# Kernel tuning notes

Measured on AMD Instinct MI355X. Metric: run time of the kernel, lower is better.

## Reference

```python
import jax, jax.numpy as jnp
import numpy as np
import math

H = 1024
N_HEADS = 16
B, S = 2, 2048

def setup_inputs() -> dict:
    key = jax.random.key(0)
    ks = jax.random.split(key, 10)
    s = 0.02
    inp = {
        "x": jax.random.normal(ks[0], (B, S, H), dtype=jnp.float32),
        "attention_mask": jnp.zeros((B, 1, 1, S), dtype=jnp.float32),
        "Wq": jax.random.normal(ks[1], (H, H), dtype=jnp.float32) * s,
        "bq": jnp.zeros((H,), dtype=jnp.float32),
        "Wk": jax.random.normal(ks[2], (H, H), dtype=jnp.float32) * s,
        "bk": jnp.zeros((H,), dtype=jnp.float32),
        "Wv": jax.random.normal(ks[3], (H, H), dtype=jnp.float32) * s,
        "bv": jnp.zeros((H,), dtype=jnp.float32),
        "Wo": jax.random.normal(ks[4], (H, H), dtype=jnp.float32) * s,
        "bo": jnp.zeros((H,), dtype=jnp.float32),
    }
    return inp

def reference(x, attention_mask, Wq, bq, Wk, bk, Wv, bv, Wo, bo):
    b, s, h = x.shape
    n = N_HEADS
    d = h // n
    scale = 1.0 / math.sqrt(h / n)
    # Linear projections (torch Linear: x @ W.T + b)
    q = (x @ Wq.T + bq).reshape(b, s, n, d).transpose(0, 2, 1, 3)  # [b,n,s,d]
    k = (x @ Wk.T + bk).reshape(b, s, n, d).transpose(0, 2, 1, 3)
    v = (x @ Wv.T + bv).reshape(b, s, n, d).transpose(0, 2, 1, 3)
    scores = jnp.einsum("bnqd,bnkd->bnqk", q, k) * scale + attention_mask
    probs = jax.nn.softmax(scores, axis=-1)
    attn = jnp.einsum("bnqk,bnkd->bnqd", probs, v)
    attn = attn.transpose(0, 2, 1, 3).reshape(b, s, h)
    return attn @ Wo.T + bo
```

## Files before the change

### kernel.cpp

```cpp
#include <hip/hip_runtime.h>

typedef __bf16 bf16;
typedef __bf16 bf16x8 __attribute__((ext_vector_type(8)));
typedef __bf16 bf16x4 __attribute__((ext_vector_type(4)));
typedef float f32x4 __attribute__((ext_vector_type(4)));
typedef float f32x16 __attribute__((ext_vector_type(16)));
typedef unsigned int u32;
typedef u32 u32x4 __attribute__((ext_vector_type(4)));
typedef const u32 __attribute__((address_space(1)))* gp1_t;
typedef u32 __attribute__((address_space(3)))* lp3_t;

constexpr int Hdim = 1024;
constexpr int SEQ  = 2048;
constexpr int NB   = 2;
constexpr int NHEAD = 16;
constexpr int DHEAD = 64;
constexpr int MR = NB * SEQ;
constexpr float LOG2E = 1.4426950408889634f;
constexpr float QSCALE = 0.125f * LOG2E;

__device__ __forceinline__ float fexp2(float x) { return __builtin_amdgcn_exp2f(x); }

__device__ __forceinline__ void gld16(const void* g, void* l) {
  __builtin_amdgcn_global_load_lds((gp1_t)g, (lp3_t)l, 16, 0, 0);
}

__device__ __forceinline__ u32 cvtpk_bf16(float lo, float hi) {
  u32 r;
  asm("v_cvt_pk_bf16_f32 %0, %1, %2" : "=v"(r) : "v"(lo), "v"(hi));
  return r;
}

__global__ __launch_bounds__(256) void cvt_all_k(
    const float* __restrict__ x, const float* __restrict__ Wq, const float* __restrict__ Wk,
    const float* __restrict__ Wv, const float* __restrict__ Wo, const float* __restrict__ mask,
    bf16* __restrict__ xb, bf16* __restrict__ wqkv, bf16* __restrict__ wob,
    bf16* __restrict__ maskB) {
  const int n8x = MR * Hdim / 8;
  const int n8w = Hdim * Hdim / 8;
  int i = blockIdx.x * 256 + threadIdx.x;
  const float* src;
  bf16* dst;
  int slot;
  if (i < n8x) {
    src = x; dst = xb; slot = i;
  } else if (i < n8x + 4 * n8w) {
    int j = i - n8x;
    int w = j >> 17;
    int o = j & (n8w - 1);
    if (w == 0)      { src = Wq; dst = wqkv;            }
    else if (w == 1) { src = Wk; dst = wqkv + (size_t)Hdim * Hdim;     }
    else if (w == 2) { src = Wv; dst = wqkv + (size_t)2 * Hdim * Hdim; }
    else             { src = Wo; dst = wob;             }
    slot = o;
  } else {
    int o = i - (n8x + 4 * n8w);
    const float4* p = reinterpret_cast<const float4*>(mask) + (size_t)o * 2;
    float4 a = p[0], b = p[1];
    bf16x8 o8;
    o8[0] = (bf16)(a.x * LOG2E); o8[1] = (bf16)(a.y * LOG2E);
    o8[2] = (bf16)(a.z * LOG2E); o8[3] = (bf16)(a.w * LOG2E);
    o8[4] = (bf16)(b.x * LOG2E); o8[5] = (bf16)(b.y * LOG2E);
    o8[6] = (bf16)(b.z * LOG2E); o8[7] = (bf16)(b.w * LOG2E);
    reinterpret_cast<bf16x8*>(maskB)[o] = o8;
    return;
  }
  const float4* p = reinterpret_cast<const float4*>(src) + (size_t)slot * 2;
  float4 a = p[0], b = p[1];
  bf16x8 o8;
  o8[0] = (bf16)a.x; o8[1] = (bf16)a.y; o8[2] = (bf16)a.z; o8[3] = (bf16)a.w;
  o8[4] = (bf16)b.x; o8[5] = (bf16)b.y; o8[6] = (bf16)b.z; o8[7] = (bf16)b.w;
  reinterpret_cast<bf16x8*>(dst)[slot] = o8;
}

__global__ __launch_bounds__(256) void qkv_gemm_k(
    const bf16* __restrict__ A, const bf16* __restrict__ Bw,
    const float* __restrict__ bq, const float* __restrict__ bk, const float* __restrict__ bv,
    bf16* __restrict__ Qw, bf16* __restrict__ Kw, bf16* __restrict__ VTw)
{
  __shared__ __align__(16) bf16 As[3][128][32];
  __shared__ __align__(16) bf16 Bs[3][128][32];

  const int t = threadIdx.x;
  const int lane = t & 63, wave = t >> 6;
  const int ql = lane & 15, g = lane >> 4;
  const int wr = wave >> 1, wc = wave & 1;
  const int row0 = blockIdx.x * 128;
  const int col0 = blockIdx.y * 128;
  const int z = blockIdx.y >> 3;
  const float* bias = (z == 0) ? bq : (z == 1) ? bk : bv;
  const int rsl = (g ^ ((ql >> 1) & 3)) * 8;

  f32x4 acc[4][4] = {};

#define STAGE_QKV(buf, kt)                                                        \
  {                                                                               \
    _Pragma("unroll")                                                             \
    for (int i = 0; i < 2; ++i) {                                                 \
      int c = i * 256 + t;                                                        \
      int r = c >> 2, sp = c & 3;                                                 \
      int sl = (sp ^ ((r >> 1) & 3)) << 3;                                        \
      gld16(&A[(size_t)(row0 + r) * Hdim + (kt) + sl], (char*)&As[buf][0][0] + c * 16); \
      gld16(&Bw[(size_t)(col0 + r) * Hdim + (kt) + sl], (char*)&Bs[buf][0][0] + c * 16); \
    }                                                                             \
  }

  constexpr int NT = Hdim / 32;
  STAGE_QKV(0, 0);
  STAGE_QKV(1, 32);

  int cur = 0;
  for (int it = 0; it < NT; ++it) {
    if (it + 2 < NT) {
      int stg = cur + 2; if (stg >= 3) stg -= 3;
      STAGE_QKV(stg, (it + 2) * 32);
      asm volatile("s_waitcnt vmcnt(8)" ::: "memory");
    } else if (it + 1 < NT) {
      asm volatile("s_waitcnt vmcnt(4)" ::: "memory");
    } else {
      asm volatile("s_waitcnt vmcnt(0)" ::: "memory");
    }
    __builtin_amdgcn_s_barrier();

    bf16x8 af[4], bfr[4];
#pragma unroll
    for (int m = 0; m < 4; ++m)
      af[m] = *reinterpret_cast<const bf16x8*>(&As[cur][wr * 64 + m * 16 + ql][rsl]);
#pragma unroll
    for (int n = 0; n < 4; ++n)
      bfr[n] = *reinterpret_cast<const bf16x8*>(&Bs[cur][wc * 64 + n * 16 + ql][rsl]);
#pragma unroll
    for (int m = 0; m < 4; ++m)
#pragma unroll
      for (int n = 0; n < 4; ++n)
        acc[m][n] = __builtin_amdgcn_mfma_f32_16x16x32_bf16(af[m], bfr[n], acc[m][n], 0, 0, 0);

    __builtin_amdgcn_s_barrier();
    cur = (cur + 1 == 3) ? 0 : cur + 1;
  }
#undef STAGE_QKV

  const float oscale = (z == 0) ? QSCALE : 1.0f;
#pragma unroll
  for (int m = 0; m < 4; ++m) {
#pragma unroll
    for (int n = 0; n < 4; ++n) {
#pragma unroll
      for (int r = 0; r < 4; ++r) {
        int gi = row0 + wr * 64 + m * 16 + g * 4 + r;
        int gj = col0 + wc * 64 + n * 16 + ql;
        int j1 = gj & (Hdim - 1);
        float v = (acc[m][n][r] + bias[j1]) * oscale;
        int b = gi >> 11, s = gi & (SEQ - 1);
        int hh = j1 >> 6, dd = j1 & 63;
        if (z == 0)
          Qw[((size_t)(b * NHEAD + hh) * SEQ + s) * DHEAD + dd] = (bf16)v;
        else if (z == 1)
          Kw[((size_t)(b * NHEAD + hh) * SEQ + s) * DHEAD + dd] = (bf16)v;
        else
          VTw[((size_t)(b * NHEAD + hh) * DHEAD + dd) * SEQ + s] = (bf16)v;
      }
    }
  }
}

__global__ __launch_bounds__(256) void attn_fwd_k(
    const bf16* __restrict__ Q, const bf16* __restrict__ K,
    const bf16* __restrict__ VT, const bf16* __restrict__ maskB,
    bf16* __restrict__ Out)
{
  const int head = blockIdx.x;
  const int qt = blockIdx.y;
  const int b = head >> 4;
  const int hh = head & 15;
  const int t = threadIdx.x, lane = t & 63, wave = t >> 6;
  const int q = lane & 31, h = lane >> 5;

  __shared__ __align__(16) bf16 Ks[2][64][64];
  __shared__ __align__(16) bf16 VTs[2][64][64];
  __shared__ __align__(16) bf16 Ms[SEQ];

  const bf16* Qh  = Q  + (size_t)head * SEQ * DHEAD;
  const bf16* Kh  = K  + (size_t)head * SEQ * DHEAD;
  const bf16* VTh = VT + (size_t)head * DHEAD * SEQ;
  const bf16* mrow = maskB + (size_t)b * SEQ;

  const int q0w = qt * 128 + wave * 32;

  bf16x8 qf[4];
#pragma unroll
  for (int s = 0; s < 4; ++s)
    qf[s] = *reinterpret_cast<const bf16x8*>(&Qh[(size_t)(q0w + q) * DHEAD + s * 16 + 8 * h]);

  f32x16 accT[2] = {};
  f32x4 psum4 = {0.f, 0.f, 0.f, 0.f};

#define STAGE_KV(buf, tile)                                                       \
  {                                                                               \
    const int nb0 = (tile) * 64;                                                  \
    _Pragma("unroll")                                                             \
    for (int i = 0; i < 2; ++i) {                                                 \
      int c = i * 256 + t, r = c >> 3, sp = c & 7, sl = sp ^ (r & 7);             \
      gld16(&Kh[(size_t)(nb0 + r) * DHEAD + sl * 8], (char*)&Ks[buf][0][0] + c * 16); \
      gld16(&VTh[(size_t)r * SEQ + nb0 + sl * 8], (char*)&VTs[buf][0][0] + c * 16);   \
    }                                                                             \
  }

  constexpr int NT = SEQ / 64;
  gld16(&mrow[t * 8], (char*)&Ms[0] + t * 16);
  STAGE_KV(0, 0);
  asm volatile("s_waitcnt vmcnt(0)" ::: "memory");
  __builtin_amdgcn_s_barrier();

  for (int it = 0; it < NT; ++it) {
    const int cur = it & 1;
    if (it + 1 < NT) STAGE_KV(cur ^ 1, it + 1);

    const char* ksb = (const char*)&Ks[cur][0][0];
    const char* vsb = (const char*)&VTs[cur][0][0];
    const int kb0 = it * 64;

    f32x16 sacc[2];
#pragma unroll
    for (int tt = 0; tt < 2; ++tt) {
#pragma unroll
      for (int s = 0; s < 4; ++s) {
        bf16x4 m4 = *reinterpret_cast<const bf16x4*>(&Ms[kb0 + 32 * tt + 8 * s + 4 * h]);
#pragma unroll
        for (int r = 0; r < 4; ++r) sacc[tt][s * 4 + r] = (float)m4[r];
      }
    }

    __builtin_amdgcn_s_setprio(1);
#pragma unroll
    for (int tt = 0; tt < 2; ++tt) {
      const int row = 32 * tt + q;
      const int rsw = (row & 7) << 4;
#pragma unroll
      for (int s = 0; s < 4; ++s) {
        bf16x8 kf = *reinterpret_cast<const bf16x8*>(ksb + row * 128 + ((32 * s + 16 * h) ^ rsw));
        sacc[tt] = __builtin_amdgcn_mfma_f32_32x32x16_bf16(kf, qf[s], sacc[tt], 0, 0, 0);
      }
    }
    __builtin_amdgcn_s_setprio(0);

    float pe[2][16];
#pragma unroll
    for (int tt = 0; tt < 2; ++tt)
#pragma unroll
      for (int i = 0; i < 16; ++i) {
        pe[tt][i] = fexp2(sacc[tt][i]);
        psum4[i & 3] += pe[tt][i];
      }

    u32x4 pw[4];
#pragma unroll
    for (int m = 0; m < 4; ++m) {
      const int tt = m >> 1, mi = (m & 1) * 8;
      u32 w0a = cvtpk_bf16(pe[tt][mi + 0], pe[tt][mi + 1]);
      u32 w0b = cvtpk_bf16(pe[tt][mi + 2], pe[tt][mi + 3]);
      u32 w1a = cvtpk_bf16(pe[tt][mi + 4], pe[tt][mi + 5]);
      u32 w1b = cvtpk_bf16(pe[tt][mi + 6], pe[tt][mi + 7]);
      asm("v_permlane32_swap_b32 %0, %1" : "+v"(w0a), "+v"(w1a));
      asm("v_permlane32_swap_b32 %0, %1" : "+v"(w0b), "+v"(w1b));
      pw[m][0] = w0a; pw[m][1] = w0b; pw[m][2] = w1a; pw[m][3] = w1b;
    }

    __builtin_amdgcn_s_setprio(1);
#pragma unroll
    for (int td = 0; td < 2; ++td) {
      const int row = 32 * td + q;
      const int rsw = (row & 7) << 4;
#pragma unroll
      for (int m = 0; m < 4; ++m) {
        bf16x8 vf = *reinterpret_cast<const bf16x8*>(vsb + row * 128 + ((32 * m + 16 * h) ^ rsw));
        bf16x8 pf = __builtin_bit_cast(bf16x8, pw[m]);
        accT[td] = __builtin_amdgcn_mfma_f32_32x32x16_bf16(vf, pf, accT[td], 0, 0, 0);
      }
    }
    __builtin_amdgcn_s_setprio(0);

    if (it + 1 < NT) asm volatile("s_waitcnt vmcnt(0)" ::: "memory");
    __builtin_amdgcn_s_barrier();
  }
#undef STAGE_KV

  float l = (psum4[0] + psum4[1]) + (psum4[2] + psum4[3]);
  l += __shfl_xor(l, 32);
  const float inv = 1.0f / l;

  char* slab = (char*)&Ks[0][0][0] + wave * 4096;
  const int qsw = (q & 7) << 4;
#pragma unroll
  for (int td = 0; td < 2; ++td)
#pragma unroll
    for (int s = 0; s < 4; ++s) {
      bf16x4 o4;
#pragma unroll
      for (int r = 0; r < 4; ++r) o4[r] = (bf16)(accT[td][s * 4 + r] * inv);
      *reinterpret_cast<bf16x4*>(slab + q * 128 + (((32 * td + 8 * s + 4 * h) * 2) ^ qsw)) = o4;
    }
  asm volatile("s_waitcnt lgkmcnt(0)" ::: "memory");
#pragma unroll
  for (int i = 0; i < 4; ++i) {
    const int row = i * 8 + (lane >> 3);
    bf16x8 v = *reinterpret_cast<const bf16x8*>(slab + row * 128 + (((lane & 7) << 4) ^ ((row & 7) << 4)));
    *reinterpret_cast<bf16x8*>(&Out[((size_t)(b * SEQ) + q0w + row) * Hdim + hh * 64 + (lane & 7) * 8]) = v;
  }
}

__global__ __launch_bounds__(256) void out_gemm_k(
    const bf16* __restrict__ A, const bf16* __restrict__ Bm,
    const float* __restrict__ bias, float* __restrict__ C)
{
  __shared__ __align__(16) bf16 As[3][128][32];
  __shared__ __align__(16) bf16 Bs[3][64][32];

  const int t = threadIdx.x;
  const int lane = t & 63, wave = t >> 6;
  const int ql = lane & 15, g = lane >> 4;
  const int wr = wave >> 1, wc = wave & 1;
  const int row0 = blockIdx.x * 128;
  const int col0 = blockIdx.y * 64;
  const int rsl = (g ^ ((ql >> 1) & 3)) * 8;

  f32x4 acc[4][2] = {};

#define STAGE_OUT(buf, kt)                                                        \
  {                                                                               \
    _Pragma("unroll")                                                             \
    for (int i = 0; i < 2; ++i) {                                                 \
      int c = i * 256 + t;                                                        \
      int r = c >> 2, sp = c & 3;                                                 \
      int sl = (sp ^ ((r >> 1) & 3)) << 3;                                        \
      gld16(&A[(size_t)(row0 + r) * Hdim + (kt) + sl], (char*)&As[buf][0][0] + c * 16); \
    }                                                                             \
    {                                                                             \
      int c = t;                                                                  \
      int r = c >> 2, sp = c & 3;                                                 \
      int sl = (sp ^ ((r >> 1) & 3)) << 3;                                        \
      gld16(&Bm[(size_t)(col0 + r) * Hdim + (kt) + sl], (char*)&Bs[buf][0][0] + c * 16); \
    }                                                                             \
  }

  constexpr int NT = Hdim / 32;
  STAGE_OUT(0, 0);
  STAGE_OUT(1, 32);

  int cur = 0;
  for (int it = 0; it < NT; ++it) {
    if (it + 2 < NT) {
      int stg = cur + 2; if (stg >= 3) stg -= 3;
      STAGE_OUT(stg, (it + 2) * 32);
      asm volatile("s_waitcnt vmcnt(6)" ::: "memory");
    } else if (it + 1 < NT) {
      asm volatile("s_waitcnt vmcnt(3)" ::: "memory");
    } else {
      asm volatile("s_waitcnt vmcnt(0)" ::: "memory");
    }
    __builtin_amdgcn_s_barrier();

    bf16x8 af[4], bfr[2];
#pragma unroll
    for (int m = 0; m < 4; ++m)
      af[m] = *reinterpret_cast<const bf16x8*>(&As[cur][wr * 64 + m * 16 + ql][rsl]);
#pragma unroll
    for (int n = 0; n < 2; ++n)
      bfr[n] = *reinterpret_cast<const bf16x8*>(&Bs[cur][wc * 32 + n * 16 + ql][rsl]);
#pragma unroll
    for (int m = 0; m < 4; ++m)
#pragma unroll
      for (int n = 0; n < 2; ++n)
        acc[m][n] = __builtin_amdgcn_mfma_f32_16x16x32_bf16(af[m], bfr[n], acc[m][n], 0, 0, 0);

    __builtin_amdgcn_s_barrier();
    cur = (cur + 1 == 3) ? 0 : cur + 1;
  }
#undef STAGE_OUT

#pragma unroll
  for (int m = 0; m < 4; ++m)
#pragma unroll
    for (int n = 0; n < 2; ++n)
#pragma unroll
      for (int r = 0; r < 4; ++r) {
        int gi = row0 + wr * 64 + m * 16 + g * 4 + r;
        int gj = col0 + wc * 32 + n * 16 + ql;
        C[(size_t)gi * Hdim + gj] = acc[m][n][r] + bias[gj];
      }
}

extern "C" void kernel_launch(void* const* d_in, const int* in_sizes, int n_in,
                              void* d_out, int out_size, void* d_ws, size_t ws_size,
                              hipStream_t stream) {
  const float* x    = (const float*)d_in[0];
  const float* mask = (const float*)d_in[1];
  const float* Wq   = (const float*)d_in[2];
  const float* bq   = (const float*)d_in[3];
  const float* Wk   = (const float*)d_in[4];
  const float* bk   = (const float*)d_in[5];
  const float* Wv   = (const float*)d_in[6];
  const float* bv   = (const float*)d_in[7];
  const float* Wo   = (const float*)d_in[8];
  const float* bo   = (const float*)d_in[9];
  float* out = (float*)d_out;

  bf16* xb   = (bf16*)d_ws;
  const size_t big = (size_t)MR * Hdim;
  bf16* wqkv = xb + big;
  bf16* wob  = wqkv + (size_t)3 * Hdim * Hdim;
  bf16* qw   = wob + (size_t)Hdim * Hdim;
  bf16* kw   = qw + big;
  bf16* vtw  = kw + big;
  bf16* attnb = vtw + big;
  bf16* maskB = attnb + big;

  const int nslots = MR * Hdim / 8 + 4 * (Hdim * Hdim / 8) + NB * SEQ / 8;
  cvt_all_k<<<nslots / 256, 256, 0, stream>>>(x, Wq, Wk, Wv, Wo, mask, xb, wqkv, wob, maskB);

  qkv_gemm_k<<<dim3(MR / 128, 3 * Hdim / 128), 256, 0, stream>>>(
      xb, wqkv, bq, bk, bv, qw, kw, vtw);

  attn_fwd_k<<<dim3(NB * NHEAD, SEQ / 128), 256, 0, stream>>>(qw, kw, vtw, maskB, attnb);

  out_gemm_k<<<dim3(MR / 128, Hdim / 64), 256, 0, stream>>>(attnb, wob, bo, out);
}
```

Measured before the change: 126.7 us.

## Triple-buffer attention K/V staging and precompute load addresses in GEMMs

After: 121.8 us. -3.9%, faster.

```diff
diff --git a/kernel.cpp b/kernel.cpp
--- a/kernel.cpp
+++ b/kernel.cpp
@@ -91,18 +91,23 @@
   const float* bias = (z == 0) ? bq : (z == 1) ? bk : bv;
   const int rsl = (g ^ ((ql >> 1) & 3)) * 8;
 
+  const int r0  = t >> 2;
+  const int sle = ((t & 3) ^ ((t >> 3) & 3)) * 8;
+  const char* aG0 = (const char*)A  + ((size_t)(row0 + r0) * Hdim + sle) * 2;
+  const char* aG1 = aG0 + (size_t)64 * Hdim * 2;
+  const char* bG0 = (const char*)Bw + ((size_t)(col0 + r0) * Hdim + sle) * 2;
+  const char* bG1 = bG0 + (size_t)64 * Hdim * 2;
+  char* asl = (char*)&As[0][0][0];
+  char* bsl = (char*)&Bs[0][0][0];
+
   f32x4 acc[4][4] = {};
 
-#define STAGE_QKV(buf, kt)                                                        \
-  {                                                                               \
-    _Pragma("unroll")                                                             \
-    for (int i = 0; i < 2; ++i) {                                                 \
-      int c = i * 256 + t;                                                        \
-      int r = c >> 2, sp = c & 3;                                                 \
-      int sl = (sp ^ ((r >> 1) & 3)) << 3;                                        \
-      gld16(&A[(size_t)(row0 + r) * Hdim + (kt) + sl], (char*)&As[buf][0][0] + c * 16); \
-      gld16(&Bw[(size_t)(col0 + r) * Hdim + (kt) + sl], (char*)&Bs[buf][0][0] + c * 16); \
-    }                                                                             \
+#define STAGE_QKV(buf, kt)                                           \
+  {                                                                  \
+    gld16(aG0 + (kt) * 2, asl + (buf) * 8192 + t * 16);              \
+    gld16(bG0 + (kt) * 2, bsl + (buf) * 8192 + t * 16);              \
+    gld16(aG1 + (kt) * 2, asl + (buf) * 8192 + 4096 + t * 16);       \
+    gld16(bG1 + (kt) * 2, bsl + (buf) * 8192 + 4096 + t * 16);       \
   }
 
   constexpr int NT = Hdim / 32;
@@ -164,7 +169,7 @@
   }
 }
 
-__global__ __launch_bounds__(256) void attn_fwd_k(
+__global__ __launch_bounds__(256, 3) void attn_fwd_k(
     const bf16* __restrict__ Q, const bf16* __restrict__ K,
     const bf16* __restrict__ VT, const bf16* __restrict__ maskB,
     bf16* __restrict__ Out)
@@ -176,8 +181,8 @@
   const int t = threadIdx.x, lane = t & 63, wave = t >> 6;
   const int q = lane & 31, h = lane >> 5;
 
-  __shared__ __align__(16) bf16 Ks[2][64][64];
-  __shared__ __align__(16) bf16 VTs[2][64][64];
+  __shared__ __align__(16) bf16 Ks[3][64][64];
+  __shared__ __align__(16) bf16 VTs[3][64][64];
   __shared__ __align__(16) bf16 Ms[SEQ];
 
   const bf16* Qh  = Q  + (size_t)head * SEQ * DHEAD;
@@ -195,29 +200,39 @@
   f32x16 accT[2] = {};
   f32x4 psum4 = {0.f, 0.f, 0.f, 0.f};
 
-#define STAGE_KV(buf, tile)                                                       \
-  {                                                                               \
-    const int nb0 = (tile) * 64;                                                  \
-    _Pragma("unroll")                                                             \
-    for (int i = 0; i < 2; ++i) {                                                 \
-      int c = i * 256 + t, r = c >> 3, sp = c & 7, sl = sp ^ (r & 7);             \
-      gld16(&Kh[(size_t)(nb0 + r) * DHEAD + sl * 8], (char*)&Ks[buf][0][0] + c * 16); \
-      gld16(&VTh[(size_t)r * SEQ + nb0 + sl * 8], (char*)&VTs[buf][0][0] + c * 16);   \
-    }                                                                             \
+  const int r0k = t >> 3;
+  const int slk = ((t & 7) ^ (r0k & 7)) * 16;
+  const char* kG0 = (const char*)Kh + (size_t)r0k * 128 + slk;
+  const char* kG1 = kG0 + 32 * 128;
+  const char* vG0 = (const char*)VTh + (size_t)r0k * (SEQ * 2) + slk;
+  const char* vG1 = vG0 + (size_t)32 * SEQ * 2;
+  char* ksl = (char*)&Ks[0][0][0];
+  char* vsl = (char*)&VTs[0][0][0];
+
+#define STAGE_KV(buf, tile)                                                   \
+  {                                                                           \
+    gld16(kG0 + (size_t)(tile) * 8192, ksl + (buf) * 8192 + t * 16);          \
+    gld16(vG0 + (size_t)(tile) * 128,  vsl + (buf) * 8192 + t * 16);          \
+    gld16(kG1 + (size_t)(tile) * 8192, ksl + (buf) * 8192 + 4096 + t * 16);   \
+    gld16(vG1 + (size_t)(tile) * 128,  vsl + (buf) * 8192 + 4096 + t * 16);   \
   }
 
   constexpr int NT = SEQ / 64;
   gld16(&mrow[t * 8], (char*)&Ms[0] + t * 16);
   STAGE_KV(0, 0);
-  asm volatile("s_waitcnt vmcnt(0)" ::: "memory");
+  STAGE_KV(1, 1);
+  asm volatile("s_waitcnt vmcnt(4)" ::: "memory");
   __builtin_amdgcn_s_barrier();
 
+  int cur = 0;
   for (int it = 0; it < NT; ++it) {
-    const int cur = it & 1;
-    if (it + 1 < NT) STAGE_KV(cur ^ 1, it + 1);
-
-    const char* ksb = (const char*)&Ks[cur][0][0];
-    const char* vsb = (const char*)&VTs[cur][0][0];
+    if (it + 2 < NT) {
+      int stg = cur + 2; if (stg >= 3) stg -= 3;
+      STAGE_KV(stg, it + 2);
+    }
+
+    const char* ksb = ksl + cur * 8192;
+    const char* vsb = vsl + cur * 8192;
     const int kb0 = it * 64;
 
     f32x16 sacc[2];
@@ -280,8 +295,10 @@
     }
     __builtin_amdgcn_s_setprio(0);
 
-    if (it + 1 < NT) asm volatile("s_waitcnt vmcnt(0)" ::: "memory");
+    if (it + 2 < NT)      asm volatile("s_waitcnt vmcnt(4)" ::: "memory");
+    else if (it + 1 < NT) asm volatile("s_waitcnt vmcnt(0)" ::: "memory");
     __builtin_amdgcn_s_barrier();
+    cur = (cur + 1 == 3) ? 0 : cur + 1;
   }
 #undef STAGE_KV
 
@@ -324,23 +341,21 @@
   const int col0 = blockIdx.y * 64;
   const int rsl = (g ^ ((ql >> 1) & 3)) * 8;
 
+  const int r0  = t >> 2;
+  const int sle = ((t & 3) ^ ((t >> 3) & 3)) * 8;
+  const char* aG0 = (const char*)A  + ((size_t)(row0 + r0) * Hdim + sle) * 2;
+  const char* aG1 = aG0 + (size_t)64 * Hdim * 2;
+  const char* bG0 = (const char*)Bm + ((size_t)(col0 + r0) * Hdim + sle) * 2;
+  char* asl = (char*)&As[0][0][0];
+  char* bsl = (char*)&Bs[0][0][0];
+
   f32x4 acc[4][2] = {};
 
-#define STAGE_OUT(buf, kt)                                                        \
-  {                                                                               \
-    _Pragma("unroll")                                                             \
-    for (int i = 0; i < 2; ++i) {                                                 \
-      int c = i * 256 + t;                                                        \
-      int r = c >> 2, sp = c & 3;                                                 \
-      int sl = (sp ^ ((r >> 1) & 3)) << 3;                                        \
-      gld16(&A[(size_t)(row0 + r) * Hdim + (kt) + sl], (char*)&As[buf][0][0] + c * 16); \
-    }                                                                             \
-    {                                                                             \
-      int c = t;                                                                  \
-      int r = c >> 2, sp = c & 3;                                                 \
-      int sl = (sp ^ ((r >> 1) & 3)) << 3;                                        \
-      gld16(&Bm[(size_t)(col0 + r) * Hdim + (kt) + sl], (char*)&Bs[buf][0][0] + c * 16); \
-    }                                                                             \
+#define STAGE_OUT(buf, kt)                                           \
+  {                                                                  \
+    gld16(aG0 + (kt) * 2, asl + (buf) * 8192 + t * 16);              \
+    gld16(aG1 + (kt) * 2, asl + (buf) * 8192 + 4096 + t * 16);       \
+    gld16(bG0 + (kt) * 2, bsl + (buf) * 4096 + t * 16);              \
   }
 
   constexpr int NT = Hdim / 32;
```
